# Kernel optimization log

Measured on AMD Instinct MI355X. Metric: run time of the kernel, lower is better.

## Reference

```python
import jax, jax.numpy as jnp
import numpy as np

N_BINS = 15
B, S, V = 2048, 3, 32000

def setup_inputs() -> dict:
    key = jax.random.key(0)
    k1, k2 = jax.random.split(key)
    logits = jax.random.normal(k1, (B, S, V), dtype=jnp.float32)
    targets = jax.random.randint(k2, (B, 4), 0, V, dtype=jnp.int64)
    return {"logits": logits, "targets": targets}

def reference(logits, targets):
    # softmax over vocab, then per-position max confidence and argmax prediction
    probs = jax.nn.softmax(logits, axis=-1)            # [B,S,V]
    p3 = probs[:, :3, :]                               # [B,3,V]
    confidences3 = jnp.max(p3, axis=2)                 # [B,3]
    preds = jnp.argmax(p3, axis=2)                     # [B,3]
    confidences = jnp.prod(confidences3, axis=1)       # [B]
    temp_t = targets[:, 1:]                            # [B,3]
    accuracies = (preds == temp_t).astype(jnp.float32) # [B,3]
    # accuracies[in_bin].mean() over a [n,3] slice == mean of per-row means
    row_acc = jnp.mean(accuracies, axis=1)             # [B]

    boundaries = jnp.linspace(0.0, 1.0, N_BINS + 1)
    lowers, uppers = boundaries[:-1], boundaries[1:]
    # vectorized binning instead of the original per-bin python loop
    in_bin = (confidences[None, :] > lowers[:, None]) & (confidences[None, :] <= uppers[:, None])  # [15,B]
    in_bin_f = in_bin.astype(jnp.float32)
    count = jnp.sum(in_bin_f, axis=1)                  # [15]
    n = jnp.float32(confidences.shape[0])
    prop_in_bin = count / n
    safe_count = jnp.maximum(count, 1.0)
    avg_conf = jnp.sum(in_bin_f * confidences[None, :], axis=1) / safe_count
    avg_acc = jnp.sum(in_bin_f * row_acc[None, :], axis=1) / safe_count
    per_bin = jnp.where(count > 0, jnp.abs(avg_conf - avg_acc) * prop_in_bin, 0.0)
    ece = jnp.sum(per_bin).reshape(1)
    return ece
```

## Files before the change

### kernel.cpp

```cpp
#include <hip/hip_runtime.h>
#include <hip/hip_bf16.h>
#include <math.h>

#define VOCAB     32000
#define BATCH     2048
#define SEQ       3
#define ROWS      (BATCH * SEQ)
#define WPB       4
#define BLOCKSZ   (WPB * 64)
#define NF4       (VOCAB / 4 / 64)
#define NBINS     15

typedef float f32x4 __attribute__((ext_vector_type(4)));

__device__ __forceinline__ void combine(float& m, float& s, int& idx,
                                        float m2, float s2, int idx2) {
    if (m2 > m)      { s = s * __expf(m - m2) + s2; m = m2; idx = idx2; }
    else if (m2 < m) { s = s + s2 * __expf(m2 - m); }
    else             { s += s2; idx = (idx2 < idx) ? idx2 : idx; }
}

__global__ __launch_bounds__(BLOCKSZ) void row_softmax_stats(
        const float* __restrict__ logits,
        float* __restrict__ maxprob,
        int*   __restrict__ amax)
{
    const int wave = threadIdx.x >> 6;
    const int lane = threadIdx.x & 63;
    const int row  = blockIdx.x * WPB + wave;
    const f32x4* base = (const f32x4*)(logits + (size_t)row * VOCAB);

    float m = -INFINITY;
    float s0 = 0.f, s1 = 0.f, s2 = 0.f, s3 = 0.f;
    int   idx = 0;

    #pragma unroll 5
    for (int i = 0; i < NF4; ++i) {
        const int f4 = lane + 64 * i;
        f32x4 v = __builtin_nontemporal_load(base + f4);
        float lm = fmaxf(fmaxf(v.x, v.y), fmaxf(v.z, v.w));
        if (lm > m) {
            float sc = __expf(m - lm);
            s0 *= sc; s1 *= sc; s2 *= sc; s3 *= sc;
            m = lm;
            idx = f4 * 4 + ((v.x == lm) ? 0 : (v.y == lm) ? 1 : (v.z == lm) ? 2 : 3);
        }
        s0 += __expf(v.x - m);
        s1 += __expf(v.y - m);
        s2 += __expf(v.z - m);
        s3 += __expf(v.w - m);
    }

    float s = (s0 + s1) + (s2 + s3);

    for (int off = 32; off > 0; off >>= 1) {
        float m2 = __shfl_down(m, off);
        float sx = __shfl_down(s, off);
        int   i2 = __shfl_down(idx, off);
        combine(m, s, idx, m2, sx, i2);
    }

    if (lane == 0) {
        maxprob[row] = 1.0f / s;
        amax[row]    = idx;
    }
}

__global__ __launch_bounds__(1024) void ece_reduce(
        const float* __restrict__ maxprob,
        const int*   __restrict__ amax,
        const int*   __restrict__ targets,
        float*       __restrict__ out)
{
    const int t = threadIdx.x;

    float c_cnt[NBINS], c_conf[NBINS], c_acc[NBINS];
    #pragma unroll
    for (int i = 0; i < NBINS; ++i) { c_cnt[i] = 0.f; c_conf[i] = 0.f; c_acc[i] = 0.f; }

    #pragma unroll
    for (int r = 0; r < BATCH / 1024; ++r) {
        const int b = t + r * 1024;
        float p0 = maxprob[b * 3 + 0];
        float p1 = maxprob[b * 3 + 1];
        float p2 = maxprob[b * 3 + 2];
        float conf = (p0 * p1) * p2;

        float acc = 0.f;
        acc += (amax[b * 3 + 0] == targets[b * 4 + 1]) ? 1.f : 0.f;
        acc += (amax[b * 3 + 1] == targets[b * 4 + 2]) ? 1.f : 0.f;
        acc += (amax[b * 3 + 2] == targets[b * 4 + 3]) ? 1.f : 0.f;
        float row_acc = acc * (1.0f / 3.0f);

        #pragma unroll
        for (int i = 0; i < NBINS; ++i) {
            float lo = (float)i       * (1.0f / 15.0f);
            float up = (float)(i + 1) * (1.0f / 15.0f);
            bool in = (conf > lo) && (conf <= up);
            if (in) { c_cnt[i] += 1.f; c_conf[i] += conf; c_acc[i] += row_acc; }
        }
    }

    #pragma unroll
    for (int i = 0; i < NBINS; ++i) {
        for (int off = 32; off > 0; off >>= 1) {
            c_cnt[i]  += __shfl_down(c_cnt[i],  off);
            c_conf[i] += __shfl_down(c_conf[i], off);
            c_acc[i]  += __shfl_down(c_acc[i],  off);
        }
    }

    __shared__ float s_cnt[NBINS], s_conf[NBINS], s_acc[NBINS];
    if (t < NBINS) { s_cnt[t] = 0.f; s_conf[t] = 0.f; s_acc[t] = 0.f; }
    __syncthreads();
    if ((t & 63) == 0) {
        #pragma unroll
        for (int i = 0; i < NBINS; ++i) {
            atomicAdd(&s_cnt[i],  c_cnt[i]);
            atomicAdd(&s_conf[i], c_conf[i]);
            atomicAdd(&s_acc[i],  c_acc[i]);
        }
    }
    __syncthreads();
    if (t == 0) {
        float ece = 0.f;
        #pragma unroll
        for (int i = 0; i < NBINS; ++i) {
            float cnt = s_cnt[i];
            if (cnt > 0.f) {
                float prop     = cnt / (float)BATCH;
                float safe_cnt = fmaxf(cnt, 1.0f);
                float avg_conf = s_conf[i] / safe_cnt;
                float avg_acc  = s_acc[i]  / safe_cnt;
                ece += fabsf(avg_conf - avg_acc) * prop;
            }
        }
        out[0] = ece;
    }
}

extern "C" void kernel_launch(void* const* d_in, const int* in_sizes, int n_in,
                              void* d_out, int out_size, void* d_ws, size_t ws_size,
                              hipStream_t stream) {
    const float* logits  = (const float*)d_in[0];
    const int*   targets = (const int*)d_in[1];
    float*       out     = (float*)d_out;

    float* maxprob = (float*)d_ws;
    int*   amax    = (int*)((char*)d_ws + ROWS * sizeof(float));

    row_softmax_stats<<<ROWS / WPB, BLOCKSZ, 0, stream>>>(logits, maxprob, amax);
    ece_reduce<<<1, 1024, 0, stream>>>(maxprob, amax, targets, out);
}
```

Before: 138.3 us.

## Fuse per-sample binning into softmax kernel with replicated atomic bin accumulators

Each block now handles one batch element, with its three sequence rows processed by three waves. The block combines the three max-probabilities and argmax hits in shared memory, then atomically adds count, confidence and accuracy into one of 8 replicated bin arrays. A tiny final kernel sums the replicas and computes the ECE. This removes the single-block reduction kernel that read the intermediate arrays, at the cost of a memset launch, global atomics and a block size of 192.

```diff
diff --git a/kernel.cpp b/kernel.cpp
--- a/kernel.cpp
+++ b/kernel.cpp
@@ -6,10 +6,11 @@
 #define BATCH     2048
 #define SEQ       3
 #define ROWS      (BATCH * SEQ)
-#define WPB       4
-#define BLOCKSZ   (WPB * 64)
+#define BLOCKSZ   (SEQ * 64)
 #define NF4       (VOCAB / 4 / 64)
 #define NBINS     15
+#define NREP      8
+#define REPSTRIDE 64
 
 typedef float f32x4 __attribute__((ext_vector_type(4)));
 
@@ -20,14 +21,15 @@
     else             { s += s2; idx = (idx2 < idx) ? idx2 : idx; }
 }
 
-__global__ __launch_bounds__(BLOCKSZ) void row_softmax_stats(
+__global__ __launch_bounds__(BLOCKSZ) void ece_fused(
         const float* __restrict__ logits,
-        float* __restrict__ maxprob,
-        int*   __restrict__ amax)
+        const int*   __restrict__ targets,
+        float*       __restrict__ bins)
 {
     const int wave = threadIdx.x >> 6;
     const int lane = threadIdx.x & 63;
-    const int row  = blockIdx.x * WPB + wave;
+    const int b    = blockIdx.x;
+    const int row  = b * SEQ + wave;
     const f32x4* base = (const f32x4*)(logits + (size_t)row * VOCAB);
 
     float m = -INFINITY;
@@ -60,83 +62,53 @@
         combine(m, s, idx, m2, sx, i2);
     }
 
-    if (lane == 0) {
-        maxprob[row] = 1.0f / s;
-        amax[row]    = idx;
+    __shared__ float p[SEQ];
+    __shared__ int   ix[SEQ];
+    if (lane == 0) { p[wave] = 1.0f / s; ix[wave] = idx; }
+    __syncthreads();
+
+    if (threadIdx.x == 0) {
+        float conf = (p[0] * p[1]) * p[2];
+        float acc = 0.f;
+        acc += (ix[0] == targets[b * 4 + 1]) ? 1.f : 0.f;
+        acc += (ix[1] == targets[b * 4 + 2]) ? 1.f : 0.f;
+        acc += (ix[2] == targets[b * 4 + 3]) ? 1.f : 0.f;
+        float row_acc = acc * (1.0f / 3.0f);
+
+        int bin = 0;
+        #pragma unroll
+        for (int k = 1; k < NBINS; ++k)
+            bin += (conf > (float)k * (1.0f / 15.0f)) ? 1 : 0;
+
+        float* rep = bins + (b & (NREP - 1)) * REPSTRIDE;
+        atomicAdd(rep + bin,          1.0f);
+        atomicAdd(rep + 16 + bin,     conf);
+        atomicAdd(rep + 32 + bin,     row_acc);
     }
 }
 
-__global__ __launch_bounds__(1024) void ece_reduce(
-        const float* __restrict__ maxprob,
-        const int*   __restrict__ amax,
-        const int*   __restrict__ targets,
+__global__ __launch_bounds__(64) void ece_final(
+        const float* __restrict__ bins,
         float*       __restrict__ out)
 {
     const int t = threadIdx.x;
-
-    float c_cnt[NBINS], c_conf[NBINS], c_acc[NBINS];
-    #pragma unroll
-    for (int i = 0; i < NBINS; ++i) { c_cnt[i] = 0.f; c_conf[i] = 0.f; c_acc[i] = 0.f; }
-
-    #pragma unroll
-    for (int r = 0; r < BATCH / 1024; ++r) {
-        const int b = t + r * 1024;
-        float p0 = maxprob[b * 3 + 0];
-        float p1 = maxprob[b * 3 + 1];
-        float p2 = maxprob[b * 3 + 2];
-        float conf = (p0 * p1) * p2;
-
-        float acc = 0.f;
-        acc += (amax[b * 3 + 0] == targets[b * 4 + 1]) ? 1.f : 0.f;
-        acc += (amax[b * 3 + 1] == targets[b * 4 + 2]) ? 1.f : 0.f;
-        acc += (amax[b * 3 + 2] == targets[b * 4 + 3]) ? 1.f : 0.f;
-        float row_acc = acc * (1.0f / 3.0f);
-
+    float per = 0.f;
+    if (t < NBINS) {
+        float cnt = 0.f, cf = 0.f, ac = 0.f;
         #pragma unroll
-        for (int i = 0; i < NBINS; ++i) {
-            float lo = (float)i       * (1.0f / 15.0f);
-            float up = (float)(i + 1) * (1.0f / 15.0f);
-            bool in = (conf > lo) && (conf <= up);
-            if (in) { c_cnt[i] += 1.f; c_conf[i] += conf; c_acc[i] += row_acc; }
+        for (int r = 0; r < NREP; ++r) {
+            cnt += bins[r * REPSTRIDE + t];
+            cf  += bins[r * REPSTRIDE + 16 + t];
+            ac  += bins[r * REPSTRIDE + 32 + t];
+        }
+        if (cnt > 0.f) {
+            float prop = cnt / (float)BATCH;
+            float safe = fmaxf(cnt, 1.0f);
+            per = fabsf(cf / safe - ac / safe) * prop;
         }
     }
-
-    #pragma unroll
-    for (int i = 0; i < NBINS; ++i) {
-        for (int off = 32; off > 0; off >>= 1) {
-            c_cnt[i]  += __shfl_down(c_cnt[i],  off);
-            c_conf[i] += __shfl_down(c_conf[i], off);
-            c_acc[i]  += __shfl_down(c_acc[i],  off);
-        }
-    }
-
-    __shared__ float s_cnt[NBINS], s_conf[NBINS], s_acc[NBINS];
-    if (t < NBINS) { s_cnt[t] = 0.f; s_conf[t] = 0.f; s_acc[t] = 0.f; }
-    __syncthreads();
-    if ((t & 63) == 0) {
-        #pragma unroll
-        for (int i = 0; i < NBINS; ++i) {
-            atomicAdd(&s_cnt[i],  c_cnt[i]);
-            atomicAdd(&s_conf[i], c_conf[i]);
-            atomicAdd(&s_acc[i],  c_acc[i]);
-        }
-    }
-    __syncthreads();
-    if (t == 0) {
-        float ece = 0.f;
-        #pragma unroll
-        for (int i = 0; i < NBINS; ++i) {
-            float cnt = s_cnt[i];
-            if (cnt > 0.f) {
-                float prop     = cnt / (float)BATCH;
-                float safe_cnt = fmaxf(cnt, 1.0f);
-                float avg_conf = s_conf[i] / safe_cnt;
-                float avg_acc  = s_acc[i]  / safe_cnt;
-                ece += fabsf(avg_conf - avg_acc) * prop;
-            }
-        }
-        out[0] = ece;
-    }
+    for (int off = 32; off > 0; off >>= 1) per += __shfl_down(per, off);
+    if (t == 0) out[0] = per;
 }
 
 extern "C" void kernel_launch(void* const* d_in, const int* in_sizes, int n_in,
@@ -145,10 +117,9 @@
     const float* logits  = (const float*)d_in[0];
     const int*   targets = (const int*)d_in[1];
     float*       out     = (float*)d_out;
+    float*       bins    = (float*)d_ws;
 
-    float* maxprob = (float*)d_ws;
-    int*   amax    = (int*)((char*)d_ws + ROWS * sizeof(float));
-
-    row_softmax_stats<<<ROWS / WPB, BLOCKSZ, 0, stream>>>(logits, maxprob, amax);
-    ece_reduce<<<1, 1024, 0, stream>>>(maxprob, amax, targets, out);
+    hipMemsetAsync(bins, 0, NREP * REPSTRIDE * sizeof(float), stream);
+    ece_fused<<<BATCH, BLOCKSZ, 0, stream>>>(logits, targets, bins);
+    ece_final<<<1, 64, 0, stream>>>(bins, out);
 }
```

New measurement: 127.2 us. 8.0% less time.
